# Kernel optimization log

Hardware: AMD Instinct MI355X
Metric: run time of the kernel (lower is better)

## Reference

```python
import jax, jax.numpy as jnp
import numpy as np

N, F_IN, H, C, E, G, OUT = 50000, 128, 4, 64, 800000, 128, 8

def _glorot(key, shape):
    lim = float(np.sqrt(6.0 / (shape[0] + shape[-1] if len(shape) == 2 else shape[-1] + 1)))
    return jax.random.uniform(key, shape, jnp.float32, -lim, lim)

def setup_inputs() -> dict:
    key = jax.random.key(0)
    ks = jax.random.split(key, 12)
    x = jax.random.normal(ks[0], (N, F_IN), jnp.float32)
    edge_index = jax.random.randint(ks[1], (2, E), 0, N, jnp.int64)
    batch = jnp.sort(jax.random.randint(ks[2], (N,), 0, G, jnp.int64))
    return {
        "x": x, "edge_index": edge_index, "batch": batch,
        "W1": _glorot(ks[3], (F_IN, H * C)),
        "a1s": _glorot(ks[4], (H, C)), "a1d": _glorot(ks[5], (H, C)),
        "b1": jnp.zeros((H * C,), jnp.float32),
        "W2": _glorot(ks[6], (H * C, H * C)),
        "a2s": _glorot(ks[7], (H, C)), "a2d": _glorot(ks[8], (H, C)),
        "b2": jnp.zeros((C,), jnp.float32),
        "fc_w": _glorot(ks[9], (C, OUT)),
        "fc_b": jnp.zeros((OUT,), jnp.float32),
    }

def _gat_conv(x, src, dst, W, a_src, a_dst, bias, concat):
    # x: [N, in]; src/dst: [E'] (self-loops already appended, PyG default)
    n = x.shape[0]
    h = (x @ W).reshape(n, H, C)                       # [N, H, C]
    alpha_src = (h * a_src).sum(-1)                    # [N, H]
    alpha_dst = (h * a_dst).sum(-1)                    # [N, H]
    e = alpha_src[src] + alpha_dst[dst]                # [E', H]
    e = jax.nn.leaky_relu(e, 0.2)
    # neighbor softmax grouped by destination node
    m = jax.ops.segment_max(e, dst, num_segments=n)    # [N, H]
    ex = jnp.exp(e - m[dst])
    denom = jax.ops.segment_sum(ex, dst, num_segments=n)
    alpha = ex / (denom[dst] + 1e-16)                  # [E', H]
    msg = h[src] * alpha[:, :, None]                   # [E', H, C]
    out = jax.ops.segment_sum(msg, dst, num_segments=n)  # [N, H, C]
    out = out.reshape(n, H * C) if concat else out.mean(axis=1)
    return out + bias

def reference(x, edge_index, batch, W1, a1s, a1d, b1, W2, a2s, a2d, b2, fc_w, fc_b):
    n = x.shape[0]
    loop = jnp.arange(n, dtype=edge_index.dtype)
    src = jnp.concatenate([edge_index[0], loop])
    dst = jnp.concatenate([edge_index[1], loop])
    h = _gat_conv(x, src, dst, W1, a1s, a1d, b1, concat=True)
    h = jax.nn.elu(h)                                  # activation, dropout p=0
    h = _gat_conv(h, src, dst, W2, a2s, a2d, b2, concat=False)
    # global mean pool over graphs
    sums = jax.ops.segment_sum(h, batch, num_segments=G)
    cnts = jax.ops.segment_sum(jnp.ones((n,), h.dtype), batch, num_segments=G)
    pooled = sums / jnp.maximum(cnts, 1.0)[:, None]    # [G, C]
    return pooled @ fc_w + fc_b                        # [G, OUT]
```

## Files before the change

kernel.cpp:

```cpp
#include <hip/hip_runtime.h>
#include <hip/hip_bf16.h>
#include <cstddef>
#include <cstdint>

#define NN 50000
#define MPAD 50048
#define F_IN 128
#define NH 4
#define NC 64
#define NE 800000
#define NG 128
#define NOUT 8
#define HC 256
#define EP (NE + NN)

typedef unsigned short ushort_t;
typedef _Float16 f16;
typedef __attribute__((ext_vector_type(8))) _Float16 f16x8;
typedef __attribute__((ext_vector_type(4))) float f32x4;

__device__ __forceinline__ float lrelu02(float x) { return x > 0.0f ? x : 0.2f * x; }
__device__ __forceinline__ float elu1(float x)    { return x > 0.0f ? x : expm1f(x); }

__device__ __forceinline__ ushort_t f2bf(float f) {
    uint32_t u = __float_as_uint(f);
    uint32_t r = u + 0x7fffu + ((u >> 16) & 1u);
    return (ushort_t)(r >> 16);
}

__device__ __forceinline__ void gld16(const void* g, void* l) {
    __builtin_amdgcn_global_load_lds(
        (const __attribute__((address_space(1))) unsigned int*)g,
        (__attribute__((address_space(3))) unsigned int*)l, 16, 0, 0);
}

__global__ void edge_hist(const int* __restrict__ edst, int* __restrict__ deg) {
    int e = blockIdx.x * blockDim.x + threadIdx.x;
    if (e >= EP) return;
    int d = (e < NE) ? edst[e] : (e - NE);
    atomicAdd(&deg[d], 1);
}

__global__ __launch_bounds__(256) void scan_p1(const int* __restrict__ deg,
                                               int* __restrict__ partials) {
    __shared__ int lds[256];
    int b = blockIdx.x, t = threadIdx.x;
    int i0 = b * 1024 + t * 4;
    int s = 0;
#pragma unroll
    for (int j = 0; j < 4; j++) { int i = i0 + j; if (i < NN) s += deg[i]; }
    lds[t] = s;
    __syncthreads();
    for (int o = 128; o; o >>= 1) { if (t < o) lds[t] += lds[t + o]; __syncthreads(); }
    if (t == 0) partials[b] = lds[0];
}

__global__ __launch_bounds__(256) void scan_p3(const int* __restrict__ deg,
                                               const int* __restrict__ partials,
                                               int* __restrict__ offs) {
    __shared__ int lds[256];
    __shared__ int base_s;
    int b = blockIdx.x, t = threadIdx.x;
    if (t == 0) {
        int s = 0;
        for (int i = 0; i < b; i++) s += partials[i];
        base_s = s;
        if (b == 0) offs[0] = 0;
    }
    int i0 = b * 1024 + t * 4;
    int v[4]; int s = 0;
#pragma unroll
    for (int j = 0; j < 4; j++) { int i = i0 + j; v[j] = (i < NN) ? deg[i] : 0; s += v[j]; }
    lds[t] = s;
    __syncthreads();
    for (int o = 1; o < 256; o <<= 1) {
        int x = (t >= o) ? lds[t - o] : 0;
        __syncthreads();
        lds[t] += x;
        __syncthreads();
    }
    int run = base_s + (lds[t] - s);
#pragma unroll
    for (int j = 0; j < 4; j++) { run += v[j]; int i = i0 + j; if (i < NN) offs[i + 1] = run; }
}

__global__ void edge_fill(const int* __restrict__ esrc, const int* __restrict__ edst,
                          const int* __restrict__ offs, int* __restrict__ fill,
                          int* __restrict__ csr) {
    int e = blockIdx.x * blockDim.x + threadIdx.x;
    if (e >= EP) return;
    int s, d;
    if (e < NE) { s = esrc[e]; d = edst[e]; } else { s = d = e - NE; }
    int pos = offs[d] + atomicAdd(&fill[d], 1);
    csr[pos] = s;
}

__global__ void split_x(const float* __restrict__ in, f16* __restrict__ out, int n4) {
    int i = blockIdx.x * blockDim.x + threadIdx.x;
    if (i >= n4) return;
    float4 v = ((const float4*)in)[i];
    f16 o[4] = {(f16)v.x, (f16)v.y, (f16)v.z, (f16)v.w};
    *(uint2*)(out + i * 4) = *(const uint2*)o;
}

__global__ void split_w(const float* __restrict__ W1, const float* __restrict__ W2,
                        f16* __restrict__ w1t, f16* __restrict__ w2t) {
    int idx = blockIdx.x * blockDim.x + threadIdx.x;
    const int n1 = F_IN * HC;
    if (idx < n1) {
        int k = idx / HC, n = idx % HC;
        w1t[n * F_IN + k] = (f16)W1[idx];
    } else if (idx < n1 + HC * HC) {
        int i2 = idx - n1;
        int k = i2 / HC, n = i2 % HC;
        w2t[n * HC + k] = (f16)W2[i2];
    }
}

__global__ __launch_bounds__(256, 2) void gemm_gat(
        const f16* __restrict__ A, const f16* __restrict__ BT,
        const float* __restrict__ a_s, const float* __restrict__ a_d,
        ushort_t* __restrict__ hbf2, float* __restrict__ asrc,
        float* __restrict__ adst, int M, int K) {
    __shared__ alignas(16) char smem[33792];
    f16* lA = (f16*)smem;
    f16* lB = (f16*)smem + 4096;

    int t = threadIdx.x;
    int wave = t >> 6, lane = t & 63;
    int wm = wave >> 1, wn = wave & 1;
    int quad = lane >> 4, l15 = lane & 15;
    int tileM = blockIdx.x * 128;
    int by = blockIdx.y;

    f32x4 acc[4][4];
#pragma unroll
    for (int f = 0; f < 4; f++)
#pragma unroll
        for (int g = 0; g < 4; g++) acc[f][g] = (f32x4){0.f, 0.f, 0.f, 0.f};

    for (int k0 = 0; k0 < K; k0 += 32) {
        __syncthreads();
#pragma unroll
        for (int i = 0; i < 2; i++) {
            int c = wave * 2 + i;
            int row = c * 16 + (lane >> 2);
            int kk = k0 + (lane & 3) * 8;
            gld16(A + (size_t)(tileM + row) * K + kk, &lA[c * 512]);
            gld16(BT + (size_t)(by * 128 + row) * K + kk, &lB[c * 512]);
        }
        __syncthreads();

        f16x8 ah[4], bh[4];
#pragma unroll
        for (int f = 0; f < 4; f++)
            ah[f] = *(const f16x8*)&lA[(wm * 64 + f * 16 + l15) * 32 + quad * 8];
#pragma unroll
        for (int g = 0; g < 4; g++)
            bh[g] = *(const f16x8*)&lB[(wn * 64 + g * 16 + l15) * 32 + quad * 8];
#pragma unroll
        for (int f = 0; f < 4; f++)
#pragma unroll
            for (int g = 0; g < 4; g++)
                acc[f][g] = __builtin_amdgcn_mfma_f32_16x16x32_f16(ah[f], bh[g], acc[f][g], 0, 0, 0);
    }

    int head = (by << 1) | wn;
    float as_v[4], ad_v[4];
#pragma unroll
    for (int g = 0; g < 4; g++) {
        as_v[g] = a_s[head * 64 + g * 16 + l15];
        ad_v[g] = a_d[head * 64 + g * 16 + l15];
    }
#pragma unroll
    for (int f = 0; f < 4; f++) {
#pragma unroll
        for (int r = 0; r < 4; r++) {
            float ps = acc[f][0][r] * as_v[0] + acc[f][1][r] * as_v[1]
                     + acc[f][2][r] * as_v[2] + acc[f][3][r] * as_v[3];
            float pd = acc[f][0][r] * ad_v[0] + acc[f][1][r] * ad_v[1]
                     + acc[f][2][r] * ad_v[2] + acc[f][3][r] * ad_v[3];
#pragma unroll
            for (int o = 1; o < 16; o <<= 1) {
                ps += __shfl_xor(ps, o);
                pd += __shfl_xor(pd, o);
            }
            int row = tileM + wm * 64 + f * 16 + quad * 4 + r;
            if (l15 == 0 && row < M) {
                asrc[row * 4 + head] = ps;
                adst[row * 4 + head] = pd;
            }
        }
    }

    __syncthreads();
    ushort_t* lC2u = (ushort_t*)smem;
    const uint32_t* lC2d = (const uint32_t*)smem;
#pragma unroll
    for (int f = 0; f < 4; f++)
#pragma unroll
        for (int g = 0; g < 4; g++)
#pragma unroll
            for (int r = 0; r < 4; r++)
                lC2u[(wm * 64 + f * 16 + quad * 4 + r) * 132 + (g * 16 + l15) * 2 + wn] =
                    f2bf(acc[f][g][r]);
    __syncthreads();
    uint32_t* hb2 = (uint32_t*)hbf2;
#pragma unroll
    for (int it = 0; it < 32; it++) {
        int row = wave * 32 + it;
        uint32_t v = lC2d[row * 66 + lane];
        hb2[(size_t)(tileM + row) * 128 + by * 64 + lane] = v;
    }
}

template <int CONCAT>
__global__ __launch_bounds__(256) void gat_agg(const ushort_t* __restrict__ hbf2,
                                               const float* __restrict__ asrc,
                                               const float* __restrict__ adst,
                                               const int* __restrict__ offs,
                                               const int* __restrict__ csr,
                                               const float* __restrict__ bias,
                                               f16* __restrict__ oh,
                                               float* __restrict__ of) {
    __shared__ float4 lw[4][64];
    int wave = threadIdx.x >> 6, lane = threadIdx.x & 63;
    int node = blockIdx.x * 4 + wave;
    if (node >= NN) return;
    int start = offs[node];
    int deg = offs[node + 1] - start;
    float4 ad = *(const float4*)(adst + node * 4);

    float w0, w1, w2, w3;
    float m0, m1, m2, m3, i0, i1, i2, i3;
    int msrc = 0;

    if (deg <= 64) {
        float t0 = -1e30f, t1 = -1e30f, t2 = -1e30f, t3 = -1e30f;
        if (lane < deg) {
            int sidx = csr[start + lane];
            float4 as = *(const float4*)(asrc + sidx * 4);
            t0 = lrelu02(as.x + ad.x);
            t1 = lrelu02(as.y + ad.y);
            t2 = lrelu02(as.z + ad.z);
            t3 = lrelu02(as.w + ad.w);
            msrc = sidx;
        }
        m0 = t0; m1 = t1; m2 = t2; m3 = t3;
#pragma unroll
        for (int o = 1; o < 64; o <<= 1) {
            m0 = fmaxf(m0, __shfl_xor(m0, o));
            m1 = fmaxf(m1, __shfl_xor(m1, o));
            m2 = fmaxf(m2, __shfl_xor(m2, o));
            m3 = fmaxf(m3, __shfl_xor(m3, o));
        }
        w0 = __expf(t0 - m0);
        w1 = __expf(t1 - m1);
        w2 = __expf(t2 - m2);
        w3 = __expf(t3 - m3);
        float s0 = w0, s1 = w1, s2 = w2, s3 = w3;
#pragma unroll
        for (int o = 1; o < 64; o <<= 1) {
            s0 += __shfl_xor(s0, o);
            s1 += __shfl_xor(s1, o);
            s2 += __shfl_xor(s2, o);
            s3 += __shfl_xor(s3, o);
        }
        i0 = 1.0f / (s0 + 1e-16f);
        i1 = 1.0f / (s1 + 1e-16f);
        i2 = 1.0f / (s2 + 1e-16f);
        i3 = 1.0f / (s3 + 1e-16f);
        w0 *= i0; w1 *= i1; w2 *= i2; w3 *= i3;
    } else {
        m0 = m1 = m2 = m3 = -1e30f;
        float s0 = 0.f, s1 = 0.f, s2 = 0.f, s3 = 0.f;
        float e0 = 0.f, e1 = 0.f, e2 = 0.f, e3 = 0.f;
        for (int j = lane; j < deg; j += 64) {
            int sidx = csr[start + j];
            float4 as = *(const float4*)(asrc + sidx * 4);
            float t0 = lrelu02(as.x + ad.x);
            float t1 = lrelu02(as.y + ad.y);
            float t2 = lrelu02(as.z + ad.z);
            float t3 = lrelu02(as.w + ad.w);
            if (j == lane) { e0 = t0; e1 = t1; e2 = t2; e3 = t3; msrc = sidx; }
            float nm;
            nm = fmaxf(m0, t0); s0 = s0 * __expf(m0 - nm) + __expf(t0 - nm); m0 = nm;
            nm = fmaxf(m1, t1); s1 = s1 * __expf(m1 - nm) + __expf(t1 - nm); m1 = nm;
            nm = fmaxf(m2, t2); s2 = s2 * __expf(m2 - nm) + __expf(t2 - nm); m2 = nm;
            nm = fmaxf(m3, t3); s3 = s3 * __expf(m3 - nm) + __expf(t3 - nm); m3 = nm;
        }
        for (int o = 32; o; o >>= 1) {
            float om, os, nm;
            om = __shfl_xor(m0, o); os = __shfl_xor(s0, o);
            nm = fmaxf(m0, om); s0 = s0 * __expf(m0 - nm) + os * __expf(om - nm); m0 = nm;
            om = __shfl_xor(m1, o); os = __shfl_xor(s1, o);
            nm = fmaxf(m1, om); s1 = s1 * __expf(m1 - nm) + os * __expf(om - nm); m1 = nm;
            om = __shfl_xor(m2, o); os = __shfl_xor(s2, o);
            nm = fmaxf(m2, om); s2 = s2 * __expf(m2 - nm) + os * __expf(om - nm); m2 = nm;
            om = __shfl_xor(m3, o); os = __shfl_xor(s3, o);
            nm = fmaxf(m3, om); s3 = s3 * __expf(m3 - nm) + os * __expf(om - nm); m3 = nm;
        }
        i0 = 1.0f / (s0 + 1e-16f);
        i1 = 1.0f / (s1 + 1e-16f);
        i2 = 1.0f / (s2 + 1e-16f);
        i3 = 1.0f / (s3 + 1e-16f);
        w0 = __expf(e0 - m0) * i0;
        w1 = __expf(e1 - m1) * i1;
        w2 = __expf(e2 - m2) * i2;
        w3 = __expf(e3 - m3) * i3;
    }

    lw[wave][lane] = (float4){w0, w1, w2, w3};

    int hp = lane >> 5;
    const float2* lwp = (const float2*)&lw[wave][0];
    float aE0 = 0.f, aO0 = 0.f, aE1 = 0.f, aO1 = 0.f;
    const uint32_t* hb = (const uint32_t*)hbf2 + lane * 2;
    int jmax = deg < 64 ? deg : 64;
#pragma unroll 8
    for (int j = 0; j < jmax; j++) {
        int sidx = __builtin_amdgcn_readlane(msrc, j);
        float2 w = lwp[j * 2 + hp];
        uint2 q = *(const uint2*)(hb + (size_t)sidx * 128);
        aE0 += w.x * __uint_as_float(q.x << 16);
        aO0 += w.y * __uint_as_float(q.x & 0xffff0000u);
        aE1 += w.x * __uint_as_float(q.y << 16);
        aO1 += w.y * __uint_as_float(q.y & 0xffff0000u);
    }
    for (int j = 64; j < deg; j++) {
        int sidx = csr[start + j];
        float4 as = *(const float4*)(asrc + sidx * 4);
        float u0 = __expf(lrelu02(as.x + ad.x) - m0) * i0;
        float u1 = __expf(lrelu02(as.y + ad.y) - m1) * i1;
        float u2 = __expf(lrelu02(as.z + ad.z) - m2) * i2;
        float u3 = __expf(lrelu02(as.w + ad.w) - m3) * i3;
        float ue = hp ? u2 : u0;
        float uo = hp ? u3 : u1;
        uint2 q = *(const uint2*)(hb + (size_t)sidx * 128);
        aE0 += ue * __uint_as_float(q.x << 16);
        aO0 += uo * __uint_as_float(q.x & 0xffff0000u);
        aE1 += ue * __uint_as_float(q.y << 16);
        aO1 += uo * __uint_as_float(q.y & 0xffff0000u);
    }

    int c0 = (lane & 31) * 2;
    int he = hp * 2, ho = hp * 2 + 1;
    if (CONCAT) {
        size_t base = (size_t)node * HC;
        float vE0 = elu1(aE0 + bias[he * 64 + c0]);
        float vE1 = elu1(aE1 + bias[he * 64 + c0 + 1]);
        float vO0 = elu1(aO0 + bias[ho * 64 + c0]);
        float vO1 = elu1(aO1 + bias[ho * 64 + c0 + 1]);
        f16 pe[2] = {(f16)vE0, (f16)vE1};
        f16 po[2] = {(f16)vO0, (f16)vO1};
        *(uint32_t*)(oh + base + he * 64 + c0) = *(const uint32_t*)pe;
        *(uint32_t*)(oh + base + ho * 64 + c0) = *(const uint32_t*)po;
    } else {
        float s0 = aE0 + aO0;
        float s1 = aE1 + aO1;
        s0 += __shfl_xor(s0, 32);
        s1 += __shfl_xor(s1, 32);
        if (hp == 0) {
            float2 v = {0.25f * s0 + bias[c0], 0.25f * s1 + bias[c0 + 1]};
            *(float2*)(of + (size_t)node * NC + c0) = v;
        }
    }
}

__global__ __launch_bounds__(256) void pool_kernel(const float* __restrict__ out2,
                                                   const int* __restrict__ batch,
                                                   float* __restrict__ pool,
                                                   float* __restrict__ cnt) {
    int gw = (blockIdx.x * blockDim.x + threadIdx.x) >> 6;
    int lane = threadIdx.x & 63;
    int start = gw * 16;
    if (start >= NN) return;
    int end = start + 16 < NN ? start + 16 : NN;
    int curg = batch[start];
    float acc = 0.f; int run = 0;
    for (int node = start; node < end; node++) {
        int g = batch[node];
        if (g != curg) {
            atomicAdd(&pool[curg * 64 + lane], acc);
            if (lane == 0) atomicAdd(&cnt[curg], (float)run);
            curg = g; acc = 0.f; run = 0;
        }
        acc += out2[(size_t)node * NC + lane];
        run++;
    }
    atomicAdd(&pool[curg * 64 + lane], acc);
    if (lane == 0) atomicAdd(&cnt[curg], (float)run);
}

__global__ void fc_kernel(const float* __restrict__ pool, const float* __restrict__ cnt,
                          const float* __restrict__ fc_w, const float* __restrict__ fc_b,
                          float* __restrict__ out) {
    int idx = blockIdx.x * blockDim.x + threadIdx.x;
    if (idx >= NG * NOUT) return;
    int g = idx >> 3, o = idx & 7;
    float inv = 1.0f / fmaxf(cnt[g], 1.0f);
    float s = 0.f;
#pragma unroll
    for (int c = 0; c < 64; c++) s += pool[g * 64 + c] * fc_w[c * 8 + o];
    out[idx] = s * inv + fc_b[o];
}

extern "C" void kernel_launch(void* const* d_in, const int* in_sizes, int n_in,
                              void* d_out, int out_size, void* d_ws, size_t ws_size,
                              hipStream_t stream) {
    const float* x    = (const float*)d_in[0];
    const int*   ei   = (const int*)d_in[1];
    const int*   batch= (const int*)d_in[2];
    const float* W1   = (const float*)d_in[3];
    const float* a1s  = (const float*)d_in[4];
    const float* a1d  = (const float*)d_in[5];
    const float* b1   = (const float*)d_in[6];
    const float* W2   = (const float*)d_in[7];
    const float* a2s  = (const float*)d_in[8];
    const float* a2d  = (const float*)d_in[9];
    const float* b2   = (const float*)d_in[10];
    const float* fc_w = (const float*)d_in[11];
    const float* fc_b = (const float*)d_in[12];
    float* out = (float*)d_out;

    char* p = (char*)d_ws;
    auto alloc = [&](size_t bytes) -> char* {
        char* r = p; p += (bytes + 255) & ~(size_t)255; return r;
    };
    int*   deg     = (int*)alloc((size_t)NN * 4);
    int*   fill    = (int*)alloc((size_t)NN * 4);
    float* pool    = (float*)alloc((size_t)NG * 64 * 4);
    float* cnt     = (float*)alloc((size_t)NG * 4);
    size_t zero_bytes = (size_t)(p - (char*)d_ws);
    int*   offs    = (int*)alloc((size_t)(NN + 1) * 4);
    int*   partials= (int*)alloc(64 * 4);
    int*   csr     = (int*)alloc((size_t)EP * 4);
    float* asrc    = (float*)alloc((size_t)NN * 4 * 4);
    float* adst    = (float*)alloc((size_t)NN * 4 * 4);
    ushort_t* hbf2 = (ushort_t*)alloc((size_t)MPAD * HC * 2);
    f16*   xh      = (f16*)alloc((size_t)MPAD * F_IN * 2);
    f16*   act     = (f16*)alloc((size_t)MPAD * HC * 2);
    f16*   w1t     = (f16*)alloc((size_t)HC * F_IN * 2);
    f16*   w2t     = (f16*)alloc((size_t)HC * HC * 2);
    float* out2    = (float*)xh;

    hipMemsetAsync(d_ws, 0, zero_bytes, stream);

    int eb = (EP + 255) / 256;
    edge_hist<<<eb, 256, 0, stream>>>(ei + NE, deg);
    scan_p1<<<49, 256, 0, stream>>>(deg, partials);
    scan_p3<<<49, 256, 0, stream>>>(deg, partials, offs);
    edge_fill<<<eb, 256, 0, stream>>>(ei, ei + NE, offs, fill, csr);

    int xn4 = NN * F_IN / 4;
    split_x<<<(xn4 + 255) / 256, 256, 0, stream>>>(x, xh, xn4);
    split_w<<<(F_IN * HC + HC * HC + 255) / 256, 256, 0, stream>>>(W1, W2, w1t, w2t);

    dim3 gg((NN + 127) / 128, HC / 128);
    int nb4 = (NN + 3) / 4;

    gemm_gat<<<gg, 256, 0, stream>>>(xh, w1t, a1s, a1d, hbf2, asrc, adst, NN, F_IN);
    gat_agg<1><<<nb4, 256, 0, stream>>>(hbf2, asrc, adst, offs, csr, b1, act, nullptr);
    gemm_gat<<<gg, 256, 0, stream>>>(act, w2t, a2s, a2d, hbf2, asrc, adst, NN, HC);
    gat_agg<0><<<nb4, 256, 0, stream>>>(hbf2, asrc, adst, offs, csr, b2, nullptr, out2);
    pool_kernel<<<((NN + 15) / 16 + 3) / 4, 256, 0, stream>>>(out2, batch, pool, cnt);
    fc_kernel<<<(NG * NOUT + 255) / 256, 256, 0, stream>>>(pool, cnt, fc_w, fc_b, out);
}
```

Measured before the change: 407.4 us.

## Fuse prep kernels, store h as fp16, raise gemm occupancy, count pool in prep

Merges the edge histogram, x and W conversion, and per-graph node counting into one prep kernel, which cuts launch count and takes the count atomics out of the pool kernel. The intermediate h is now stored as fp16 instead of bf16, so unpacking uses f16-to-f32 conversions rather than shifts. gemm_gat launch bounds go from 2 to 3 blocks per SM, which may force register spilling. The fp16 storage keeps more mantissa but has a narrower range.

New measurement: 535.6 us. +31.5%, slower.

```diff
diff --git a/kernel.cpp b/kernel.cpp
--- a/kernel.cpp
+++ b/kernel.cpp
@@ -22,10 +22,15 @@
 __device__ __forceinline__ float lrelu02(float x) { return x > 0.0f ? x : 0.2f * x; }
 __device__ __forceinline__ float elu1(float x)    { return x > 0.0f ? x : expm1f(x); }
 
-__device__ __forceinline__ ushort_t f2bf(float f) {
-    uint32_t u = __float_as_uint(f);
-    uint32_t r = u + 0x7fffu + ((u >> 16) & 1u);
-    return (ushort_t)(r >> 16);
+__device__ __forceinline__ ushort_t f2h_bits(float f) {
+    f16 h = (f16)f;
+    union { f16 h; ushort_t u; } cv; cv.h = h;
+    return cv.u;
+}
+__device__ __forceinline__ void h2_unpack(uint32_t q, float& lo, float& hi) {
+    union { uint32_t u; f16 h[2]; } cv; cv.u = q;
+    lo = (float)cv.h[0];
+    hi = (float)cv.h[1];
 }
 
 __device__ __forceinline__ void gld16(const void* g, void* l) {
@@ -34,11 +39,44 @@
         (__attribute__((address_space(3))) unsigned int*)l, 16, 0, 0);
 }
 
-__global__ void edge_hist(const int* __restrict__ edst, int* __restrict__ deg) {
-    int e = blockIdx.x * blockDim.x + threadIdx.x;
-    if (e >= EP) return;
-    int d = (e < NE) ? edst[e] : (e - NE);
-    atomicAdd(&deg[d], 1);
+#define XN4 (NN * F_IN / 4)
+#define NW (F_IN * HC + HC * HC)
+__global__ void prep_kernel(const int* __restrict__ edst,
+                            const int* __restrict__ batch,
+                            const float* __restrict__ x,
+                            const float* __restrict__ W1,
+                            const float* __restrict__ W2,
+                            int* __restrict__ deg, float* __restrict__ cnt,
+                            f16* __restrict__ xh,
+                            f16* __restrict__ w1t, f16* __restrict__ w2t) {
+    int idx = blockIdx.x * blockDim.x + threadIdx.x;
+    if (idx < EP) {
+        int d = (idx < NE) ? edst[idx] : (idx - NE);
+        atomicAdd(&deg[d], 1);
+        return;
+    }
+    idx -= EP;
+    if (idx < NN) {
+        atomicAdd(&cnt[batch[idx]], 1.0f);
+        return;
+    }
+    idx -= NN;
+    if (idx < XN4) {
+        float4 v = ((const float4*)x)[idx];
+        f16 o[4] = {(f16)v.x, (f16)v.y, (f16)v.z, (f16)v.w};
+        *(uint2*)(xh + idx * 4) = *(const uint2*)o;
+        return;
+    }
+    idx -= XN4;
+    const int n1 = F_IN * HC;
+    if (idx < n1) {
+        int k = idx / HC, n = idx % HC;
+        w1t[n * F_IN + k] = (f16)W1[idx];
+    } else if (idx < NW) {
+        int i2 = idx - n1;
+        int k = i2 / HC, n = i2 % HC;
+        w2t[n * HC + k] = (f16)W2[i2];
+    }
 }
 
 __global__ __launch_bounds__(256) void scan_p1(const int* __restrict__ deg,
@@ -95,32 +133,10 @@
     csr[pos] = s;
 }
 
-__global__ void split_x(const float* __restrict__ in, f16* __restrict__ out, int n4) {
-    int i = blockIdx.x * blockDim.x + threadIdx.x;
-    if (i >= n4) return;
-    float4 v = ((const float4*)in)[i];
-    f16 o[4] = {(f16)v.x, (f16)v.y, (f16)v.z, (f16)v.w};
-    *(uint2*)(out + i * 4) = *(const uint2*)o;
-}
-
-__global__ void split_w(const float* __restrict__ W1, const float* __restrict__ W2,
-                        f16* __restrict__ w1t, f16* __restrict__ w2t) {
-    int idx = blockIdx.x * blockDim.x + threadIdx.x;
-    const int n1 = F_IN * HC;
-    if (idx < n1) {
-        int k = idx / HC, n = idx % HC;
-        w1t[n * F_IN + k] = (f16)W1[idx];
-    } else if (idx < n1 + HC * HC) {
-        int i2 = idx - n1;
-        int k = i2 / HC, n = i2 % HC;
-        w2t[n * HC + k] = (f16)W2[i2];
-    }
-}
-
-__global__ __launch_bounds__(256, 2) void gemm_gat(
+__global__ __launch_bounds__(256, 3) void gemm_gat(
         const f16* __restrict__ A, const f16* __restrict__ BT,
         const float* __restrict__ a_s, const float* __restrict__ a_d,
-        ushort_t* __restrict__ hbf2, float* __restrict__ asrc,
+        ushort_t* __restrict__ hf2, float* __restrict__ asrc,
         float* __restrict__ adst, int M, int K) {
     __shared__ alignas(16) char smem[33792];
     f16* lA = (f16*)smem;
@@ -203,9 +219,9 @@
 #pragma unroll
             for (int r = 0; r < 4; r++)
                 lC2u[(wm * 64 + f * 16 + quad * 4 + r) * 132 + (g * 16 + l15) * 2 + wn] =
-                    f2bf(acc[f][g][r]);
+                    f2h_bits(acc[f][g][r]);
     __syncthreads();
-    uint32_t* hb2 = (uint32_t*)hbf2;
+    uint32_t* hb2 = (uint32_t*)hf2;
 #pragma unroll
     for (int it = 0; it < 32; it++) {
         int row = wave * 32 + it;
@@ -215,7 +231,7 @@
 }
 
 template <int CONCAT>
-__global__ __launch_bounds__(256) void gat_agg(const ushort_t* __restrict__ hbf2,
+__global__ __launch_bounds__(256) void gat_agg(const ushort_t* __restrict__ hf2,
                                                const float* __restrict__ asrc,
                                                const float* __restrict__ adst,
                                                const int* __restrict__ offs,
@@ -315,17 +331,20 @@
     int hp = lane >> 5;
     const float2* lwp = (const float2*)&lw[wave][0];
     float aE0 = 0.f, aO0 = 0.f, aE1 = 0.f, aO1 = 0.f;
-    const uint32_t* hb = (const uint32_t*)hbf2 + lane * 2;
+    const uint32_t* hb = (const uint32_t*)hf2 + lane * 2;
     int jmax = deg < 64 ? deg : 64;
 #pragma unroll 8
     for (int j = 0; j < jmax; j++) {
         int sidx = __builtin_amdgcn_readlane(msrc, j);
         float2 w = lwp[j * 2 + hp];
         uint2 q = *(const uint2*)(hb + (size_t)sidx * 128);
-        aE0 += w.x * __uint_as_float(q.x << 16);
-        aO0 += w.y * __uint_as_float(q.x & 0xffff0000u);
-        aE1 += w.x * __uint_as_float(q.y << 16);
-        aO1 += w.y * __uint_as_float(q.y & 0xffff0000u);
+        float xl, xh2, yl, yh;
+        h2_unpack(q.x, xl, xh2);
+        h2_unpack(q.y, yl, yh);
+        aE0 += w.x * xl;
+        aO0 += w.y * xh2;
+        aE1 += w.x * yl;
+        aO1 += w.y * yh;
     }
     for (int j = 64; j < deg; j++) {
         int sidx = csr[start + j];
@@ -337,10 +356,13 @@
         float ue = hp ? u2 : u0;
         float uo = hp ? u3 : u1;
         uint2 q = *(const uint2*)(hb + (size_t)sidx * 128);
-        aE0 += ue * __uint_as_float(q.x << 16);
-        aO0 += uo * __uint_as_float(q.x & 0xffff0000u);
-        aE1 += ue * __uint_as_float(q.y << 16);
-        aO1 += uo * __uint_as_float(q.y & 0xffff0000u);
+        float xl, xh2, yl, yh;
+        h2_unpack(q.x, xl, xh2);
+        h2_unpack(q.y, yl, yh);
+        aE0 += ue * xl;
+        aO0 += uo * xh2;
+        aE1 += ue * yl;
+        aO1 += uo * yh;
     }
 
     int c0 = (lane & 31) * 2;
@@ -369,27 +391,23 @@
 
 __global__ __launch_bounds__(256) void pool_kernel(const float* __restrict__ out2,
                                                    const int* __restrict__ batch,
-                                                   float* __restrict__ pool,
-                                                   float* __restrict__ cnt) {
+                                                   float* __restrict__ pool) {
     int gw = (blockIdx.x * blockDim.x + threadIdx.x) >> 6;
     int lane = threadIdx.x & 63;
     int start = gw * 16;
     if (start >= NN) return;
     int end = start + 16 < NN ? start + 16 : NN;
     int curg = batch[start];
-    float acc = 0.f; int run = 0;
+    float acc = 0.f;
     for (int node = start; node < end; node++) {
         int g = batch[node];
         if (g != curg) {
             atomicAdd(&pool[curg * 64 + lane], acc);
-            if (lane == 0) atomicAdd(&cnt[curg], (float)run);
-            curg = g; acc = 0.f; run = 0;
+            curg = g; acc = 0.f;
         }
         acc += out2[(size_t)node * NC + lane];
-        run++;
     }
     atomicAdd(&pool[curg * 64 + lane], acc);
-    if (lane == 0) atomicAdd(&cnt[curg], (float)run);
 }
 
 __global__ void fc_kernel(const float* __restrict__ pool, const float* __restrict__ cnt,
@@ -437,7 +455,7 @@
     int*   csr     = (int*)alloc((size_t)EP * 4);
     float* asrc    = (float*)alloc((size_t)NN * 4 * 4);
     float* adst    = (float*)alloc((size_t)NN * 4 * 4);
-    ushort_t* hbf2 = (ushort_t*)alloc((size_t)MPAD * HC * 2);
+    ushort_t* hf2  = (ushort_t*)alloc((size_t)MPAD * HC * 2);
     f16*   xh      = (f16*)alloc((size_t)MPAD * F_IN * 2);
     f16*   act     = (f16*)alloc((size_t)MPAD * HC * 2);
     f16*   w1t     = (f16*)alloc((size_t)HC * F_IN * 2);
@@ -446,23 +464,20 @@
 
     hipMemsetAsync(d_ws, 0, zero_bytes, stream);
 
-    int eb = (EP + 255) / 256;
-    edge_hist<<<eb, 256, 0, stream>>>(ei + NE, deg);
+    int prep_n = EP + NN + XN4 + NW;
+    prep_kernel<<<(prep_n + 255) / 256, 256, 0, stream>>>(
+        ei + NE, batch, x, W1, W2, deg, cnt, xh, w1t, w2t);
     scan_p1<<<49, 256, 0, stream>>>(deg, partials);
     scan_p3<<<49, 256, 0, stream>>>(deg, partials, offs);
-    edge_fill<<<eb, 256, 0, stream>>>(ei, ei + NE, offs, fill, csr);
-
-    int xn4 = NN * F_IN / 4;
-    split_x<<<(xn4 + 255) / 256, 256, 0, stream>>>(x, xh, xn4);
-    split_w<<<(F_IN * HC + HC * HC + 255) / 256, 256, 0, stream>>>(W1, W2, w1t, w2t);
+    edge_fill<<<(EP + 255) / 256, 256, 0, stream>>>(ei, ei + NE, offs, fill, csr);
 
     dim3 gg((NN + 127) / 128, HC / 128);
     int nb4 = (NN + 3) / 4;
 
-    gemm_gat<<<gg, 256, 0, stream>>>(xh, w1t, a1s, a1d, hbf2, asrc, adst, NN, F_IN);
-    gat_agg<1><<<nb4, 256, 0, stream>>>(hbf2, asrc, adst, offs, csr, b1, act, nullptr);
-    gemm_gat<<<gg, 256, 0, stream>>>(act, w2t, a2s, a2d, hbf2, asrc, adst, NN, HC);
-    gat_agg<0><<<nb4, 256, 0, stream>>>(hbf2, asrc, adst, offs, csr, b2, nullptr, out2);
-    pool_kernel<<<((NN + 15) / 16 + 3) / 4, 256, 0, stream>>>(out2, batch, pool, cnt);
+    gemm_gat<<<gg, 256, 0, stream>>>(xh, w1t, a1s, a1d, hf2, asrc, adst, NN, F_IN);
+    gat_agg<1><<<nb4, 256, 0, stream>>>(hf2, asrc, adst, offs, csr, b1, act, nullptr);
+    gemm_gat<<<gg, 256, 0, stream>>>(act, w2t, a2s, a2d, hf2, asrc, adst, NN, HC);
+    gat_agg<0><<<nb4, 256, 0, stream>>>(hf2, asrc, adst, offs, csr, b2, nullptr, out2);
+    pool_kernel<<<((NN + 15) / 16 + 3) / 4, 256, 0, stream>>>(out2, batch, pool);
     fc_kernel<<<(NG * NOUT + 255) / 256, 256, 0, stream>>>(pool, cnt, fc_w, fc_b, out);
 }
```
